# Kernel optimization log

Measured on AMD Instinct MI355X. Metric: run time of the kernel, lower is better.

## Reference

```python
import jax, jax.numpy as jnp
import numpy as np


def setup_inputs() -> dict:
    key = jax.random.key(0)
    k1, k2, k3, k4 = jax.random.split(key, 4)
    B, S, E, D = 8, 2048, 1024, 64
    return {
        "sequence": jax.random.normal(k1, (B, S, E), dtype=jnp.float32),
        "Wk": jax.random.normal(k2, (E, D), dtype=jnp.float32) * (E ** -0.5),
        "Wq": jax.random.normal(k3, (E, D), dtype=jnp.float32) * (E ** -0.5),
        "Wv": jax.random.normal(k4, (E, D), dtype=jnp.float32) * (E ** -0.5),
    }


def reference(sequence, Wk, Wq, Wv):
    # sequence: [B, S, E]; Wk/Wq/Wv: [E, D]
    B, S, E = sequence.shape
    D = Wk.shape[-1]
    k = sequence @ Wk  # [B, S, D]
    q = sequence @ Wq  # [B, S, D]
    v = sequence @ Wv  # [B, S, D]
    scores = jnp.einsum("bqd,bkd->bqk", q, k) * (D ** -0.5)  # [B, S, S]
    causal = jnp.tril(jnp.ones((S, S), dtype=bool))
    scores = jnp.where(causal, scores, -jnp.inf)
    attn = jax.nn.softmax(scores, axis=-1)  # [B, S, S]
    out = jnp.einsum("bqk,bkd->bqd", attn, v)  # [B, S, D]
    return (out, attn)
```

## Files before the change

kernel.cpp:

```cpp
#include <hip/hip_runtime.h>
#include <hip/hip_bf16.h>


typedef __attribute__((ext_vector_type(8))) __bf16 bf16x8;
typedef __attribute__((ext_vector_type(4))) float f32x4;

constexpr int S_LEN = 2048;

__device__ inline unsigned short f2bf(float f) {
  union { float f; unsigned u; } v; v.f = f;
  unsigned u = v.u + 0x7FFFu + ((v.u >> 16) & 1u);
  return (unsigned short)(u >> 16);
}

__device__ inline uint4 pack8u(float4 f0, float4 f1) {
  union { __hip_bfloat162 h[4]; uint4 v; } u;
  u.h[0] = __float22bfloat162_rn(float2{f0.x, f0.y});
  u.h[1] = __float22bfloat162_rn(float2{f0.z, f0.w});
  u.h[2] = __float22bfloat162_rn(float2{f1.x, f1.y});
  u.h[3] = __float22bfloat162_rn(float2{f1.z, f1.w});
  return u.v;
}

__global__ __launch_bounds__(256) void wt_conv(
    const float* __restrict__ Wq, const float* __restrict__ Wk,
    const float* __restrict__ Wv, unsigned short* __restrict__ wt) {
  __shared__ float T[64][65];
  const int mat = blockIdx.y;
  const int k0 = blockIdx.x * 64;
  const float* W = (mat == 0) ? Wq : ((mat == 1) ? Wk : Wv);
  const int t = threadIdx.x;

  for (int s = 0; s < 4; ++s) {
    int rr = (t >> 4) + s * 16;
    int cc = (t & 15) * 4;
    float4 f = *(const float4*)(W + (size_t)(k0 + rr) * 64 + cc);
    T[rr][cc] = f.x; T[rr][cc + 1] = f.y; T[rr][cc + 2] = f.z; T[rr][cc + 3] = f.w;
  }
  __syncthreads();
  const float sc = (mat == 0) ? 0.125f : 1.0f;
  const int n = t >> 2, kc = (t & 3) * 16;
  union { unsigned short s[16]; uint4 v[2]; } tmp;
  for (int i = 0; i < 16; ++i) tmp.s[i] = f2bf(T[kc + i][n] * sc);
  unsigned short* dst = wt + (size_t)(mat * 64 + n) * 1024 + k0 + kc;
  *(uint4*)dst = tmp.v[0];
  *(uint4*)(dst + 8) = tmp.v[1];
}

__global__ __launch_bounds__(256) void qkv_gemm(
    const float* __restrict__ seq, const unsigned short* __restrict__ wt,
    unsigned short* __restrict__ qb, unsigned short* __restrict__ kb,
    unsigned short* __restrict__ vt) {
  __shared__ unsigned short As[2][32][72];
  const int row0 = blockIdx.x * 32;
  const int t = threadIdx.x;
  const int wv = t >> 6, lane = t & 63, lm = lane & 15, lq = lane >> 4;

  f32x4 acc[6];
  for (int i = 0; i < 6; ++i) acc[i] = (f32x4){0.f, 0.f, 0.f, 0.f};

  const int srow = t >> 3, skc = (t & 7) * 8;
  const float* ap = seq + (size_t)(row0 + srow) * 1024 + skc;

  float4 f0 = *(const float4*)ap;
  float4 f1 = *(const float4*)(ap + 4);
  *(uint4*)&As[0][srow][skc] = pack8u(f0, f1);

  for (int i = 0; i < 16; ++i) {
    if (i < 15) {
      f0 = *(const float4*)(ap + (i + 1) * 64);
      f1 = *(const float4*)(ap + (i + 1) * 64 + 4);
    }
    __syncthreads();
    const int buf = i & 1;
    for (int ks = 0; ks < 2; ++ks) {
      bf16x8 a0 = *(const bf16x8*)&As[buf][lm][ks * 32 + lq * 8];
      bf16x8 a1 = *(const bf16x8*)&As[buf][16 + lm][ks * 32 + lq * 8];
      for (int nt = 0; nt < 3; ++nt) {
        const unsigned short* bp =
            wt + (size_t)(wv * 48 + nt * 16 + lm) * 1024 + i * 64 + ks * 32 + lq * 8;
        bf16x8 bfr = *(const bf16x8*)bp;
        acc[nt] = __builtin_amdgcn_mfma_f32_16x16x32_bf16(a0, bfr, acc[nt], 0, 0, 0);
        acc[3 + nt] = __builtin_amdgcn_mfma_f32_16x16x32_bf16(a1, bfr, acc[3 + nt], 0, 0, 0);
      }
    }
    if (i < 15) *(uint4*)&As[buf ^ 1][srow][skc] = pack8u(f0, f1);
  }

  const int bb = row0 >> 11;
  const int s0 = row0 & (S_LEN - 1);
  for (int nt = 0; nt < 3; ++nt) {
    int ng = wv * 48 + nt * 16 + lm;
    int mat = ng >> 6, d = ng & 63;
    for (int mt = 0; mt < 2; ++mt) {
      f32x4 v = acc[mt * 3 + nt];
      if (mat == 2) {
        ushort4 u;
        u.x = f2bf(v[0]); u.y = f2bf(v[1]); u.z = f2bf(v[2]); u.w = f2bf(v[3]);
        *(ushort4*)(vt + ((size_t)(bb * 64 + d)) * S_LEN + s0 + mt * 16 + lq * 4) = u;
      } else {
        unsigned short* dst = mat ? kb : qb;
        for (int r = 0; r < 4; ++r)
          dst[(size_t)(row0 + mt * 16 + lq * 4 + r) * 64 + d] = f2bf(v[r]);
      }
    }
  }
}

__global__ __launch_bounds__(256) void attn_stats(
    const unsigned short* __restrict__ qb, const unsigned short* __restrict__ kb,
    float* __restrict__ lbuf) {
  __shared__ unsigned short Ks[128][72];
  const int q0 = blockIdx.x * 64, c0 = blockIdx.y * 512, b = blockIdx.z;
  if (c0 >= q0 + 64) return;
  const int kend = min(c0 + 512, q0 + 64);
  const int t = threadIdx.x, wv = t >> 6, lane = t & 63, lm = lane & 15, lq = lane >> 4;

  const unsigned short* qp = qb + ((size_t)(b * S_LEN + q0 + wv * 16 + lm)) * 64 + lq * 8;
  bf16x8 qf0 = *(const bf16x8*)qp;
  bf16x8 qf1 = *(const bf16x8*)(qp + 32);
  const int rw0 = q0 + wv * 16;

  float lp[4] = {0.f, 0.f, 0.f, 0.f};
  const int sr = t >> 3, sc = (t & 7) * 8;

  for (int kk = c0; kk < kend; kk += 128) {
    __syncthreads();
    const unsigned short* src = kb + ((size_t)(b * S_LEN + kk)) * 64;
    for (int j = 0; j < 4; ++j)
      *(uint4*)&Ks[j * 32 + sr][sc] = *(const uint4*)(src + (size_t)(j * 32 + sr) * 64 + sc);
    __syncthreads();
    if (kk <= rw0 + 15) {
      int ktmax = min(8, (rw0 + 15 - kk) / 16 + 1);
      for (int kt = 0; kt < ktmax; ++kt) {
        int key = kk + kt * 16 + lm;
        f32x4 z = (f32x4){0.f, 0.f, 0.f, 0.f};
        bf16x8 k0 = *(const bf16x8*)&Ks[kt * 16 + lm][lq * 8];
        bf16x8 k1 = *(const bf16x8*)&Ks[kt * 16 + lm][32 + lq * 8];
        z = __builtin_amdgcn_mfma_f32_16x16x32_bf16(qf0, k0, z, 0, 0, 0);
        z = __builtin_amdgcn_mfma_f32_16x16x32_bf16(qf1, k1, z, 0, 0, 0);
        for (int r = 0; r < 4; ++r) {
          float e = __expf(z[r]);
          lp[r] += (key <= rw0 + lq * 4 + r) ? e : 0.f;
        }
      }
    }
  }
  for (int off = 1; off < 16; off <<= 1)
    for (int r = 0; r < 4; ++r) lp[r] += __shfl_xor(lp[r], off);
  if (lm == 0)
    for (int r = 0; r < 4; ++r)
      unsafeAtomicAdd(&lbuf[b * S_LEN + rw0 + lq * 4 + r], lp[r]);
}

__global__ __launch_bounds__(256) void attn_write(
    const unsigned short* __restrict__ qb, const unsigned short* __restrict__ kb,
    const unsigned short* __restrict__ vt, const float* __restrict__ lbuf,
    float* __restrict__ outp, float* __restrict__ attnp) {
  __shared__ unsigned short Ks[256][72];
  __shared__ unsigned short Ps[4][16][72];
  const int q0 = blockIdx.x * 64, c0 = blockIdx.y * 256, b = blockIdx.z;
  const int t = threadIdx.x, wv = t >> 6, lane = t & 63, lm = lane & 15, lq = lane >> 4;
  float* arow = attnp + (size_t)b * S_LEN * S_LEN;

  if (c0 >= q0 + 64) {
    const int col = (t & 63) * 4, r0 = t >> 6;
    float4 z4 = {0.f, 0.f, 0.f, 0.f};
    for (int rr = r0; rr < 64; rr += 4)
      *(float4*)(arow + (size_t)(q0 + rr) * S_LEN + c0 + col) = z4;
    return;
  }

  {
    const int sr = t >> 3, sc = (t & 7) * 8;
    const unsigned short* src = kb + ((size_t)(b * S_LEN + c0)) * 64;
    for (int j = 0; j < 8; ++j)
      *(uint4*)&Ks[j * 32 + sr][sc] = *(const uint4*)(src + (size_t)(j * 32 + sr) * 64 + sc);
  }
  const unsigned short* qp = qb + ((size_t)(b * S_LEN + q0 + wv * 16 + lm)) * 64 + lq * 8;
  bf16x8 qf0 = *(const bf16x8*)qp;
  bf16x8 qf1 = *(const bf16x8*)(qp + 32);
  const int rw0 = q0 + wv * 16;
  const int row = rw0 + lm;

  const float il = 1.0f / lbuf[b * S_LEN + row];

  f32x4 o[4];
  for (int i = 0; i < 4; ++i) o[i] = (f32x4){0.f, 0.f, 0.f, 0.f};
  __syncthreads();

  for (int st = 0; st < 4; ++st) {
    const int kk0 = c0 + st * 64;
    if (kk0 > rw0 + 15) {
      float4 z4 = {0.f, 0.f, 0.f, 0.f};
      for (int r4 = 0; r4 < 4; ++r4)
        *(float4*)(arow + (size_t)(rw0 + r4 * 4 + lq) * S_LEN + kk0 + lm * 4) = z4;
      continue;
    }
    f32x4 c4[4];
#pragma unroll
    for (int kt = 0; kt < 4; ++kt) {
      bf16x8 k0 = *(const bf16x8*)&Ks[st * 64 + kt * 16 + lm][lq * 8];
      bf16x8 k1 = *(const bf16x8*)&Ks[st * 64 + kt * 16 + lm][32 + lq * 8];
      f32x4 z = (f32x4){0.f, 0.f, 0.f, 0.f};
      z = __builtin_amdgcn_mfma_f32_16x16x32_bf16(k0, qf0, z, 0, 0, 0);
      z = __builtin_amdgcn_mfma_f32_16x16x32_bf16(k1, qf1, z, 0, 0, 0);
      c4[kt] = z;
    }
    bf16x8 vf[2][4];
    for (int ks2 = 0; ks2 < 2; ++ks2)
      for (int nt = 0; nt < 4; ++nt)
        vf[ks2][nt] = *(const bf16x8*)(vt + ((size_t)(b * 64 + nt * 16 + lm)) * S_LEN +
                                       kk0 + ks2 * 32 + lq * 8);
#pragma unroll
    for (int kt = 0; kt < 4; ++kt) {
      const int keyb = kk0 + kt * 16 + lq * 4;
      float4 p;
      p.x = (keyb + 0 > row) ? 0.f : __expf(c4[kt][0]) * il;
      p.y = (keyb + 1 > row) ? 0.f : __expf(c4[kt][1]) * il;
      p.z = (keyb + 2 > row) ? 0.f : __expf(c4[kt][2]) * il;
      p.w = (keyb + 3 > row) ? 0.f : __expf(c4[kt][3]) * il;
      *(float4*)(arow + (size_t)row * S_LEN + keyb) = p;
      union { __hip_bfloat162 h[2]; ushort4 u; } pk;
      pk.h[0] = __float22bfloat162_rn(float2{p.x, p.y});
      pk.h[1] = __float22bfloat162_rn(float2{p.z, p.w});
      *(ushort4*)&Ps[wv][lm][kt * 16 + lq * 4] = pk.u;
    }
    for (int ks2 = 0; ks2 < 2; ++ks2) {
      bf16x8 pa = *(const bf16x8*)&Ps[wv][lm][ks2 * 32 + lq * 8];
      for (int nt = 0; nt < 4; ++nt)
        o[nt] = __builtin_amdgcn_mfma_f32_16x16x32_bf16(pa, vf[ks2][nt], o[nt], 0, 0, 0);
    }
  }

  for (int nt = 0; nt < 4; ++nt)
    for (int r = 0; r < 4; ++r)
      unsafeAtomicAdd(outp + ((size_t)(b * S_LEN + rw0 + lq * 4 + r)) * 64 + nt * 16 + lm,
                      o[nt][r]);
}

extern "C" void kernel_launch(void* const* d_in, const int* in_sizes, int n_in,
                              void* d_out, int out_size, void* d_ws, size_t ws_size,
                              hipStream_t stream) {
  const float* seq = (const float*)d_in[0];
  const float* Wk  = (const float*)d_in[1];
  const float* Wq  = (const float*)d_in[2];
  const float* Wv  = (const float*)d_in[3];

  float* outp = (float*)d_out;
  float* attnp = outp + (size_t)8 * S_LEN * 64;

  unsigned short* qb = (unsigned short*)d_ws;
  unsigned short* kb = qb + (size_t)16384 * 64;
  unsigned short* vt = kb + (size_t)16384 * 64;
  unsigned short* wt = vt + (size_t)8 * 64 * S_LEN;
  float* lbuf = (float*)(wt + (size_t)192 * 1024);

  hipMemsetAsync(lbuf, 0, (size_t)16384 * 4, stream);
  hipMemsetAsync(outp, 0, (size_t)8 * S_LEN * 64 * 4, stream);

  wt_conv<<<dim3(16, 3), 256, 0, stream>>>(Wq, Wk, Wv, wt);
  qkv_gemm<<<dim3(512, 1), 256, 0, stream>>>(seq, wt, qb, kb, vt);
  attn_stats<<<dim3(32, 4, 8), 256, 0, stream>>>(qb, kb, lbuf);
  attn_write<<<dim3(32, 8, 8), 256, 0, stream>>>(qb, kb, vt, lbuf, outp, attnp);
}
```

Before: 250.8 us.

## Stage full A row-block in LDS and fold output zeroing into QKV GEMM

The QKV GEMM now converts and stores the whole 32x1024 input tile to shared memory up front, with deeper register prefetch, and then runs the MFMA loop without per-iteration barriers. The two hipMemsetAsync calls are removed, and the zeroing of the output and lbuf buffers moves into the GEMM kernel. This cuts launch overhead and barrier stalls. The cost is about 66KB of LDS per block, which lowers occupancy, and the global loads are no longer overlapped with compute.

```diff
diff --git a/kernel.cpp b/kernel.cpp
--- a/kernel.cpp
+++ b/kernel.cpp
@@ -50,41 +50,69 @@
 __global__ __launch_bounds__(256) void qkv_gemm(
     const float* __restrict__ seq, const unsigned short* __restrict__ wt,
     unsigned short* __restrict__ qb, unsigned short* __restrict__ kb,
-    unsigned short* __restrict__ vt) {
-  __shared__ unsigned short As[2][32][72];
+    unsigned short* __restrict__ vt, float* __restrict__ outp,
+    float* __restrict__ lbuf) {
+  __shared__ unsigned short As[32][1032];
   const int row0 = blockIdx.x * 32;
   const int t = threadIdx.x;
   const int wv = t >> 6, lane = t & 63, lm = lane & 15, lq = lane >> 4;
 
+  {
+    uint4 z = {0u, 0u, 0u, 0u};
+    char* op = (char*)outp + ((size_t)blockIdx.x * 256 + t) * 32;
+    *(uint4*)op = z;
+    *(uint4*)(op + 16) = z;
+    if (blockIdx.x < 8) {
+      char* lp = (char*)lbuf + ((size_t)blockIdx.x * 256 + t) * 32;
+      *(uint4*)lp = z;
+      *(uint4*)(lp + 16) = z;
+    }
+  }
+
+  const int srow = t >> 3, skc = (t & 7) * 8;
+  const float* ap = seq + (size_t)(row0 + srow) * 1024 + skc;
+  float4 cur[4][2], nxt[4][2];
+#pragma unroll
+  for (int s = 0; s < 4; ++s) {
+    cur[s][0] = *(const float4*)(ap + s * 64);
+    cur[s][1] = *(const float4*)(ap + s * 64 + 4);
+  }
+#pragma unroll
+  for (int g = 0; g < 4; ++g) {
+    if (g < 3) {
+#pragma unroll
+      for (int s = 0; s < 4; ++s) {
+        nxt[s][0] = *(const float4*)(ap + (g + 1) * 256 + s * 64);
+        nxt[s][1] = *(const float4*)(ap + (g + 1) * 256 + s * 64 + 4);
+      }
+    }
+#pragma unroll
+    for (int s = 0; s < 4; ++s)
+      *(uint4*)&As[srow][(g * 4 + s) * 64 + skc] = pack8u(cur[s][0], cur[s][1]);
+    if (g < 3) {
+#pragma unroll
+      for (int s = 0; s < 4; ++s) { cur[s][0] = nxt[s][0]; cur[s][1] = nxt[s][1]; }
+    }
+  }
+
   f32x4 acc[6];
   for (int i = 0; i < 6; ++i) acc[i] = (f32x4){0.f, 0.f, 0.f, 0.f};
 
-  const int srow = t >> 3, skc = (t & 7) * 8;
-  const float* ap = seq + (size_t)(row0 + srow) * 1024 + skc;
-
-  float4 f0 = *(const float4*)ap;
-  float4 f1 = *(const float4*)(ap + 4);
-  *(uint4*)&As[0][srow][skc] = pack8u(f0, f1);
-
+  __syncthreads();
+
+  const unsigned short* wb = wt + (size_t)(wv * 48 + lm) * 1024 + lq * 8;
+#pragma unroll 4
   for (int i = 0; i < 16; ++i) {
-    if (i < 15) {
-      f0 = *(const float4*)(ap + (i + 1) * 64);
-      f1 = *(const float4*)(ap + (i + 1) * 64 + 4);
-    }
-    __syncthreads();
-    const int buf = i & 1;
     for (int ks = 0; ks < 2; ++ks) {
-      bf16x8 a0 = *(const bf16x8*)&As[buf][lm][ks * 32 + lq * 8];
-      bf16x8 a1 = *(const bf16x8*)&As[buf][16 + lm][ks * 32 + lq * 8];
+      const int col = i * 64 + ks * 32 + lq * 8;
+      bf16x8 a0 = *(const bf16x8*)&As[lm][col];
+      bf16x8 a1 = *(const bf16x8*)&As[16 + lm][col];
       for (int nt = 0; nt < 3; ++nt) {
-        const unsigned short* bp =
-            wt + (size_t)(wv * 48 + nt * 16 + lm) * 1024 + i * 64 + ks * 32 + lq * 8;
-        bf16x8 bfr = *(const bf16x8*)bp;
+        bf16x8 bfr = *(const bf16x8*)(wb + (size_t)nt * 16 * 1024 + i * 64 + ks * 32);
         acc[nt] = __builtin_amdgcn_mfma_f32_16x16x32_bf16(a0, bfr, acc[nt], 0, 0, 0);
         acc[3 + nt] = __builtin_amdgcn_mfma_f32_16x16x32_bf16(a1, bfr, acc[3 + nt], 0, 0, 0);
       }
     }
-    if (i < 15) *(uint4*)&As[buf ^ 1][srow][skc] = pack8u(f0, f1);
   }
 
   const int bb = row0 >> 11;
@@ -256,11 +284,8 @@
   unsigned short* wt = vt + (size_t)8 * 64 * S_LEN;
   float* lbuf = (float*)(wt + (size_t)192 * 1024);
 
-  hipMemsetAsync(lbuf, 0, (size_t)16384 * 4, stream);
-  hipMemsetAsync(outp, 0, (size_t)8 * S_LEN * 64 * 4, stream);
-
   wt_conv<<<dim3(16, 3), 256, 0, stream>>>(Wq, Wk, Wv, wt);
-  qkv_gemm<<<dim3(512, 1), 256, 0, stream>>>(seq, wt, qb, kb, vt);
+  qkv_gemm<<<dim3(512, 1), 256, 0, stream>>>(seq, wt, qb, kb, vt, outp, lbuf);
   attn_stats<<<dim3(32, 4, 8), 256, 0, stream>>>(qb, kb, lbuf);
   attn_write<<<dim3(32, 8, 8), 256, 0, stream>>>(qb, kb, vt, lbuf, outp, attnp);
 }
```

Measured after the change: 254.8 us. Within noise of the previous version (+1.6%).
